# Kernel optimization log

Hardware: AMD Instinct MI355X
Metric: run time of the kernel (lower is better)

Reference implementation:

```python
import jax, jax.numpy as jnp
import numpy as np

# Transformer_E (depth=1): Residual(PreNorm(MultiScaleRetention)) + Residual1(PreNorm1(FeedForward))
# MultiScaleRetention follows the standard RetNet parallel form, adapted to two inputs
# (Q from x, K/V from z) as implied by PreNorm passing both normed streams to fn.

B, S, DIM, HEADS, MLP = 16, 1024, 256, 4, 512
HEAD = DIM // HEADS  # per-head qkv size; v_dim = DIM
EPS = 1e-5           # torch LayerNorm/GroupNorm default eps


def _ln(x, w, b):
    mu = jnp.mean(x, -1, keepdims=True)
    var = jnp.mean((x - mu) ** 2, -1, keepdims=True)
    return (x - mu) * jax.lax.rsqrt(var + EPS) * w + b


def _decay_matrix():
    # RetNet gammas: 1 - exp(linspace(log(1/32), log(1/512), heads))
    gammas = 1.0 - jnp.exp(jnp.linspace(jnp.log(1.0 / 32.0), jnp.log(1.0 / 512.0), HEADS))
    n = jnp.arange(S)
    diff = (n[:, None] - n[None, :]).astype(jnp.float32)  # [S,S]
    causal = diff >= 0
    D = jnp.where(causal[None], gammas[:, None, None] ** diff[None], 0.0)  # [H,S,S]
    return D.astype(jnp.float32)


def setup_inputs() -> dict:
    key = jax.random.key(0)
    ks = jax.random.split(key, 9)
    s = 1.0 / DIM  # repo inits W as randn/hidden_size
    return {
        "x": jax.random.normal(ks[0], (B, S, DIM), jnp.float32),
        "y": jax.random.normal(ks[1], (B, S, DIM), jnp.float32),
        "ln1_w": jnp.ones((DIM,), jnp.float32),
        "ln1_b": jnp.zeros((DIM,), jnp.float32),
        "W_Q": jax.random.normal(ks[2], (HEADS, DIM, HEAD), jnp.float32) * s,
        "W_K": jax.random.normal(ks[3], (HEADS, DIM, HEAD), jnp.float32) * s,
        "W_V": jax.random.normal(ks[4], (HEADS, DIM, HEAD), jnp.float32) * s,
        "gn_w": jnp.ones((DIM,), jnp.float32),
        "gn_b": jnp.zeros((DIM,), jnp.float32),
        "W_G": jax.random.normal(ks[5], (DIM, DIM), jnp.float32) * s,
        "W_O": jax.random.normal(ks[6], (DIM, DIM), jnp.float32) * s,
        "ln2_w": jnp.ones((DIM,), jnp.float32),
        "ln2_b": jnp.zeros((DIM,), jnp.float32),
        "ff_w1": jax.random.normal(ks[7], (DIM, MLP), jnp.float32) * (DIM ** -0.5),
        "ff_b1": jnp.zeros((MLP,), jnp.float32),
        "ff_w2": jax.random.normal(ks[8], (MLP, DIM), jnp.float32) * (MLP ** -0.5),
        "ff_b2": jnp.zeros((DIM,), jnp.float32),
    }


def reference(x, y, ln1_w, ln1_b, W_Q, W_K, W_V, gn_w, gn_b, W_G, W_O,
              ln2_w, ln2_b, ff_w1, ff_b1, ff_w2, ff_b2):
    # PreNorm: x.real -> float (already real float32 here), shared LayerNorm on both streams
    xn = _ln(x, ln1_w, ln1_b)
    zn = _ln(y, ln1_w, ln1_b)

    # --- MultiScaleRetention (parallel form) ---
    Q = jnp.einsum('bsd,hde->bhse', xn, W_Q)
    K = jnp.einsum('bsd,hde->bhse', zn, W_K)
    V = jnp.einsum('bsd,hde->bhse', zn, W_V)
    D = _decay_matrix()                                       # [H,S,S] causal decay
    scores = jnp.einsum('bhne,bhme->bhnm', Q, K) * D[None]    # [B,H,S,S]
    Yh = jnp.einsum('bhnm,bhme->bhne', scores, V)             # [B,H,S,HEAD]

    # GroupNorm(heads, v_dim) applied token-wise: normalize each head slice
    mu = jnp.mean(Yh, -1, keepdims=True)
    var = jnp.mean((Yh - mu) ** 2, -1, keepdims=True)
    Yn = (Yh - mu) * jax.lax.rsqrt(var + EPS)
    Ycat = jnp.transpose(Yn, (0, 2, 1, 3)).reshape(x.shape[0], x.shape[1], DIM)
    Ycat = Ycat * gn_w + gn_b

    # swish gate + output projection
    g = xn @ W_G
    attn_out = ((g * jax.nn.sigmoid(g)) * Ycat) @ W_O

    x1 = attn_out + x                                         # Residual

    # --- FeedForward block (Residual1(PreNorm1(FFN))) ---
    x1n = _ln(x1, ln2_w, ln2_b)
    h = jax.nn.leaky_relu(x1n @ ff_w1 + ff_b1, negative_slope=0.01)
    ff = h @ ff_w2 + ff_b2
    return ff + x1
```

## Files before the change

### kernel.cpp

```cpp
#include <hip/hip_runtime.h>

typedef float f32x4 __attribute__((ext_vector_type(4)));
typedef short bf16x8 __attribute__((ext_vector_type(8)));
typedef short s16x8 __attribute__((ext_vector_type(8)));

__device__ __forceinline__ unsigned short f2bf(float f) {
  unsigned int u = __builtin_bit_cast(unsigned int, f);
  u += 0x7fffu + ((u >> 16) & 1u);
  return (unsigned short)(u >> 16);
}
__device__ __forceinline__ float bf2f(unsigned short s) {
  unsigned int u = ((unsigned int)s) << 16;
  return __builtin_bit_cast(float, u);
}

__device__ __forceinline__ void gll16(const void* src, void* dst) {
  __builtin_amdgcn_global_load_lds((const __attribute__((address_space(1))) void*)src,
                                   (__attribute__((address_space(3))) void*)dst, 16, 0, 0);
}

__global__ __launch_bounds__(256) void prep(
    const float* __restrict__ x, const float* __restrict__ y,
    const float* __restrict__ ln1w, const float* __restrict__ ln1b,
    const float* __restrict__ WQ, const float* __restrict__ WK,
    const float* __restrict__ WV, const float* __restrict__ WG,
    const float* __restrict__ WO, const float* __restrict__ F1,
    const float* __restrict__ F2,
    unsigned short* __restrict__ XN, unsigned short* __restrict__ ZN,
    unsigned short* __restrict__ qg, unsigned short* __restrict__ kv,
    unsigned short* __restrict__ wo, unsigned short* __restrict__ f1,
    unsigned short* __restrict__ f2)
{
  const int id = blockIdx.x;
  if (id < 8192) {
    const float* X = (id < 4096) ? x : y;
    unsigned short* Y = (id < 4096) ? XN : ZN;
    const int bid = id & 4095;
    const int lane = threadIdx.x & 63;
    const size_t row = (size_t)bid * 4 + (threadIdx.x >> 6);
    const float4 v = *reinterpret_cast<const float4*>(X + row * 256 + lane * 4);
    float s = v.x + v.y + v.z + v.w;
    #pragma unroll
    for (int off = 1; off < 64; off <<= 1) s += __shfl_xor(s, off);
    float mean = s * (1.0f / 256.0f);
    float dx = v.x - mean, dy = v.y - mean, dz = v.z - mean, dw = v.w - mean;
    float q = dx * dx + dy * dy + dz * dz + dw * dw;
    #pragma unroll
    for (int off = 1; off < 64; off <<= 1) q += __shfl_xor(q, off);
    float rstd = rsqrtf(q * (1.0f / 256.0f) + 1e-5f);
    float4 wv = *reinterpret_cast<const float4*>(ln1w + lane * 4);
    float4 bv = *reinterpret_cast<const float4*>(ln1b + lane * 4);
    ushort4 o;
    o.x = f2bf(dx * rstd * wv.x + bv.x);
    o.y = f2bf(dy * rstd * wv.y + bv.y);
    o.z = f2bf(dz * rstd * wv.z + bv.z);
    o.w = f2bf(dw * rstd * wv.w + bv.w);
    *reinterpret_cast<ushort4*>(Y + row * 256 + lane * 4) = o;
    return;
  }
  int i = (id - 8192) * 256 + threadIdx.x;
  if (i < 131072) {
    int n = i >> 8, d = i & 255;
    float v = (n < 256) ? WQ[((n >> 6) * 256 + d) * 64 + (n & 63)]
                        : WG[d * 256 + (n - 256)];
    qg[i] = f2bf(v);
  } else if (i < 262144) {
    int j = i - 131072; int n = j >> 8, d = j & 255;
    float v = (n < 256) ? WK[((n >> 6) * 256 + d) * 64 + (n & 63)]
                        : WV[(((n - 256) >> 6) * 256 + d) * 64 + ((n - 256) & 63)];
    kv[j] = f2bf(v);
  } else if (i < 327680) {
    int j = i - 262144; int n = j >> 8, d = j & 255;
    wo[j] = f2bf(WO[d * 256 + n]);
  } else if (i < 458752) {
    int j = i - 327680; int n = j >> 8, d = j & 255;
    f1[j] = f2bf(F1[d * 512 + n]);
  } else if (i < 589824) {
    int j = i - 458752; int n = j >> 9, k = j & 511;
    f2[j] = f2bf(F2[k * 256 + n]);
  }
}

__global__ __launch_bounds__(256) void gemm_qkvg(
    const unsigned short* __restrict__ XN, const unsigned short* __restrict__ ZN,
    const unsigned short* __restrict__ WQG, const unsigned short* __restrict__ WKV,
    unsigned short* __restrict__ QB, unsigned short* __restrict__ GB,
    unsigned short* __restrict__ KB, unsigned short* __restrict__ VT,
    unsigned short* __restrict__ KTS)
{
  __shared__ __align__(16) char sA[2][16384];
  __shared__ __align__(16) char sB[2][8192];
  const int tid = threadIdx.x, lane = tid & 63, w = tid >> 6;
  const int z = blockIdx.z;
  const unsigned short* A = z ? ZN : XN;
  const unsigned short* Bw = z ? WKV : WQG;
  const int flat = blockIdx.x + 8 * blockIdx.y;
  const int c = flat & 7, jj = flat >> 3;
  const int m0 = (c * 16 + (jj & 15)) * 128;
  const int n0 = (jj >> 4) * 64;
  const int wr = (w >> 1) * 64, wc = (w & 1) * 32;
  const char* Ab = (const char*)A + (size_t)m0 * 512;
  const char* Bb = (const char*)Bw + (size_t)n0 * 512;
  const int srow = lane >> 3;
  const int soff = 16 * ((lane & 7) ^ srow);
  f32x4 acc[4][2] = {};

  auto stage = [&](int bufi, int kt) {
    #pragma unroll
    for (int p = 0; p < 4; ++p) {
      int row = p * 32 + w * 8 + srow;
      gll16(Ab + (size_t)row * 512 + kt + soff, &sA[bufi][p * 4096 + w * 1024]);
    }
    #pragma unroll
    for (int p = 0; p < 2; ++p) {
      int row = p * 32 + w * 8 + srow;
      gll16(Bb + (size_t)row * 512 + kt + soff, &sB[bufi][p * 4096 + w * 1024]);
    }
  };

  stage(0, 0);
  asm volatile("s_waitcnt vmcnt(0)" ::: "memory");
  __syncthreads();
  int buf = 0;
  for (int kt = 0; kt < 512; kt += 128) {
    if (kt + 128 < 512) stage(buf ^ 1, kt + 128);
    #pragma unroll
    for (int kk = 0; kk < 2; ++kk) {
      const int ib = kk * 64 + ((lane >> 4) * 16);
      bf16x8 af[4], bfr[2];
      #pragma unroll
      for (int rf = 0; rf < 4; ++rf) {
        int row = wr + rf * 16 + (lane & 15);
        af[rf] = *reinterpret_cast<const bf16x8*>(&sA[buf][row * 128 + (ib ^ ((row & 7) << 4))]);
      }
      #pragma unroll
      for (int cf = 0; cf < 2; ++cf) {
        int row = wc + cf * 16 + (lane & 15);
        bfr[cf] = *reinterpret_cast<const bf16x8*>(&sB[buf][row * 128 + (ib ^ ((row & 7) << 4))]);
      }
      #pragma unroll
      for (int rf = 0; rf < 4; ++rf)
        #pragma unroll
        for (int cf = 0; cf < 2; ++cf)
          acc[rf][cf] = __builtin_amdgcn_mfma_f32_16x16x32_bf16(af[rf], bfr[cf], acc[rf][cf], 0, 0, 0);
    }
    asm volatile("s_waitcnt vmcnt(0)" ::: "memory");
    __syncthreads();
    buf ^= 1;
  }

  const float la = logf(1.0f / 32.0f), lb = logf(1.0f / 512.0f);
  #pragma unroll
  for (int rf = 0; rf < 4; ++rf) {
    #pragma unroll
    for (int cf = 0; cf < 2; ++cf) {
      const int r0 = m0 + wr + rf * 16 + ((lane >> 4) * 4);
      const int col = n0 + wc + cf * 16 + (lane & 15);
      f32x4 v = acc[rf][cf];
      if (z == 0) {
        unsigned short* dst = (n0 < 256) ? QB : GB;
        int ccol = col & 255;
        #pragma unroll
        for (int j = 0; j < 4; ++j) dst[(size_t)(r0 + j) * 256 + ccol] = f2bf(v[j]);
      } else {
        if (n0 < 256) {
          #pragma unroll
          for (int j = 0; j < 4; ++j) KB[(size_t)(r0 + j) * 256 + col] = f2bf(v[j]);
          int hh2 = col >> 6, kd = col & 63;
          float gam = 1.0f - expf(la + (lb - la) * ((float)hh2 * (1.0f / 3.0f)));
          float lgh = log2f(gam);
          int tokc = r0 & 63;
          float scl = exp2f(lgh * (float)(64 - tokc));
          float gstep = exp2f(-lgh);
          ushort4 ks;
          ks.x = f2bf(v[0] * scl); scl *= gstep;
          ks.y = f2bf(v[1] * scl); scl *= gstep;
          ks.z = f2bf(v[2] * scl); scl *= gstep;
          ks.w = f2bf(v[3] * scl);
          int bh2 = (r0 >> 10) * 4 + hh2;
          *reinterpret_cast<ushort4*>(KTS + ((size_t)bh2 * 64 + kd) * 1024 + (r0 & 1023)) = ks;
        } else {
          int vc = col - 256, hh = vc >> 6, e = vc & 63;
          int bh = (r0 >> 10) * 4 + hh, s0 = r0 & 1023;
          ushort4 pk;
          pk.x = f2bf(v[0]); pk.y = f2bf(v[1]); pk.z = f2bf(v[2]); pk.w = f2bf(v[3]);
          *reinterpret_cast<ushort4*>(VT + (((size_t)bh * 64 + e) << 10) + s0) = pk;
        }
      }
    }
  }
}

template<int EPI>
__global__ __launch_bounds__(256) void gemm_nt(
    const unsigned short* __restrict__ A, const unsigned short* __restrict__ Bw,
    int K, unsigned short* __restrict__ o0,
    const float* __restrict__ bias, const float* __restrict__ resid,
    float* __restrict__ of)
{
  __shared__ __align__(16) char sA[2][16384];
  __shared__ __align__(16) char sB[2][8192];
  const int tid = threadIdx.x, lane = tid & 63, w = tid >> 6;
  const int flat = blockIdx.x + gridDim.x * blockIdx.y;
  const int c = flat & 7, jj = flat >> 3;
  const int m0 = (c * 16 + (jj & 15)) * 128;
  const int n0 = (jj >> 4) * 64;
  const int wr = (w >> 1) * 64, wc = (w & 1) * 32;
  const int K2 = K * 2;
  const char* Ab = (const char*)A + (size_t)m0 * K2;
  const char* Bb = (const char*)Bw + (size_t)n0 * K2;
  const int srow = lane >> 3;
  const int soff = 16 * ((lane & 7) ^ srow);
  f32x4 acc[4][2] = {};

  auto stage = [&](int bufi, int kt) {
    #pragma unroll
    for (int p = 0; p < 4; ++p) {
      int row = p * 32 + w * 8 + srow;
      gll16(Ab + (size_t)row * K2 + kt + soff, &sA[bufi][p * 4096 + w * 1024]);
    }
    #pragma unroll
    for (int p = 0; p < 2; ++p) {
      int row = p * 32 + w * 8 + srow;
      gll16(Bb + (size_t)row * K2 + kt + soff, &sB[bufi][p * 4096 + w * 1024]);
    }
  };

  stage(0, 0);
  asm volatile("s_waitcnt vmcnt(0)" ::: "memory");
  __syncthreads();
  int buf = 0;
  for (int kt = 0; kt < K2; kt += 128) {
    if (kt + 128 < K2) stage(buf ^ 1, kt + 128);
    #pragma unroll
    for (int kk = 0; kk < 2; ++kk) {
      const int ib = kk * 64 + ((lane >> 4) * 16);
      bf16x8 af[4], bfr[2];
      #pragma unroll
      for (int rf = 0; rf < 4; ++rf) {
        int row = wr + rf * 16 + (lane & 15);
        af[rf] = *reinterpret_cast<const bf16x8*>(&sA[buf][row * 128 + (ib ^ ((row & 7) << 4))]);
      }
      #pragma unroll
      for (int cf = 0; cf < 2; ++cf) {
        int row = wc + cf * 16 + (lane & 15);
        bfr[cf] = *reinterpret_cast<const bf16x8*>(&sB[buf][row * 128 + (ib ^ ((row & 7) << 4))]);
      }
      #pragma unroll
      for (int rf = 0; rf < 4; ++rf)
        #pragma unroll
        for (int cf = 0; cf < 2; ++cf)
          acc[rf][cf] = __builtin_amdgcn_mfma_f32_16x16x32_bf16(af[rf], bfr[cf], acc[rf][cf], 0, 0, 0);
    }
    asm volatile("s_waitcnt vmcnt(0)" ::: "memory");
    __syncthreads();
    buf ^= 1;
  }

  #pragma unroll
  for (int rf = 0; rf < 4; ++rf) {
    #pragma unroll
    for (int cf = 0; cf < 2; ++cf) {
      const int r0 = m0 + wr + rf * 16 + ((lane >> 4) * 4);
      const int col = n0 + wc + cf * 16 + (lane & 15);
      f32x4 v = acc[rf][cf];
      if constexpr (EPI == 3) {
        float bc = bias[col];
        #pragma unroll
        for (int j = 0; j < 4; ++j) {
          float t = v[j] + bc;
          o0[(size_t)(r0 + j) * 512 + col] = f2bf(t >= 0.0f ? t : 0.01f * t);
        }
      } else {
        float bc = bias[col];
        #pragma unroll
        for (int j = 0; j < 4; ++j) {
          size_t idx = (size_t)(r0 + j) * 256 + col;
          of[idx] = v[j] + bc + resid[idx];
        }
      }
    }
  }
}

__global__ __launch_bounds__(256) void gemm_wo_ln(
    const unsigned short* __restrict__ AY, const unsigned short* __restrict__ WoT,
    const float* __restrict__ x, const float* __restrict__ ln2w,
    const float* __restrict__ ln2b,
    float* __restrict__ X1, unsigned short* __restrict__ X1N)
{
  __shared__ __align__(16) char sA[2][4096];
  __shared__ __align__(16) char sB[2][32768];
  __shared__ float redS[32][4], redQ[32][4];
  const int tid = threadIdx.x, lane = tid & 63, w = tid >> 6;
  const int id = blockIdx.x;
  const int c = id & 7, j5 = id >> 3;
  const int m0 = (c * 64 + j5) * 32;
  const char* Ab = (const char*)AY + (size_t)m0 * 512;
  const char* Bb = (const char*)WoT;
  const int srow = lane >> 3;
  const int soff = 16 * ((lane & 7) ^ srow);
  f32x4 acc[2][4] = {};

  auto stage = [&](int bufi, int kt) {
    {
      int row = w * 8 + srow;
      gll16(Ab + (size_t)row * 512 + kt + soff, &sA[bufi][w * 1024]);
    }
    #pragma unroll
    for (int p = 0; p < 8; ++p) {
      int row = w * 64 + p * 8 + srow;
      gll16(Bb + (size_t)row * 512 + kt + soff, &sB[bufi][w * 8192 + p * 1024]);
    }
  };

  stage(0, 0);
  asm volatile("s_waitcnt vmcnt(0)" ::: "memory");
  __syncthreads();
  int buf = 0;
  for (int kt = 0; kt < 512; kt += 128) {
    if (kt + 128 < 512) stage(buf ^ 1, kt + 128);
    #pragma unroll
    for (int kk = 0; kk < 2; ++kk) {
      const int ib = kk * 64 + ((lane >> 4) * 16);
      bf16x8 af[2], bfr[4];
      #pragma unroll
      for (int mf = 0; mf < 2; ++mf) {
        int row = mf * 16 + (lane & 15);
        af[mf] = *reinterpret_cast<const bf16x8*>(&sA[buf][row * 128 + (ib ^ ((row & 7) << 4))]);
      }
      #pragma unroll
      for (int nf = 0; nf < 4; ++nf) {
        int row = w * 64 + nf * 16 + (lane & 15);
        bfr[nf] = *reinterpret_cast<const bf16x8*>(&sB[buf][row * 128 + (ib ^ ((row & 7) << 4))]);
      }
      #pragma unroll
      for (int mf = 0; mf < 2; ++mf)
        #pragma unroll
        for (int nf = 0; nf < 4; ++nf)
          acc[mf][nf] = __builtin_amdgcn_mfma_f32_16x16x32_bf16(af[mf], bfr[nf], acc[mf][nf], 0, 0, 0);
    }
    asm volatile("s_waitcnt vmcnt(0)" ::: "memory");
    __syncthreads();
    buf ^= 1;
  }

  #pragma unroll
  for (int mf = 0; mf < 2; ++mf) {
    #pragma unroll
    for (int j = 0; j < 4; ++j) {
      const int rowg = m0 + mf * 16 + ((lane >> 4) * 4) + j;
      float s = 0.0f, q = 0.0f;
      #pragma unroll
      for (int nf = 0; nf < 4; ++nf) {
        const int col = w * 64 + nf * 16 + (lane & 15);
        float v = acc[mf][nf][j] + x[(size_t)rowg * 256 + col];
        acc[mf][nf][j] = v;
        s += v; q += v * v;
      }
      #pragma unroll
      for (int off = 1; off < 16; off <<= 1) { s += __shfl_xor(s, off); q += __shfl_xor(q, off); }
      if ((lane & 15) == 0) {
        int rl = mf * 16 + ((lane >> 4) * 4) + j;
        redS[rl][w] = s; redQ[rl][w] = q;
      }
    }
  }
  __syncthreads();
  #pragma unroll
  for (int mf = 0; mf < 2; ++mf) {
    #pragma unroll
    for (int j = 0; j < 4; ++j) {
      const int rl = mf * 16 + ((lane >> 4) * 4) + j;
      const int rowg = m0 + rl;
      float sm = redS[rl][0] + redS[rl][1] + redS[rl][2] + redS[rl][3];
      float sq = redQ[rl][0] + redQ[rl][1] + redQ[rl][2] + redQ[rl][3];
      float mean = sm * (1.0f / 256.0f);
      float var = sq * (1.0f / 256.0f) - mean * mean;
      float rstd = rsqrtf(var + 1e-5f);
      #pragma unroll
      for (int nf = 0; nf < 4; ++nf) {
        const int col = w * 64 + nf * 16 + (lane & 15);
        float v = acc[mf][nf][j];
        X1[(size_t)rowg * 256 + col] = v;
        X1N[(size_t)rowg * 256 + col] = f2bf((v - mean) * rstd * ln2w[col] + ln2b[col]);
      }
    }
  }
}

__global__ __launch_bounds__(256) void calc_u(
    const unsigned short* __restrict__ KTS, const unsigned short* __restrict__ VT,
    float* __restrict__ UT)
{
  const int tid = threadIdx.x, lane = tid & 63, w = tid >> 6;
  const int id = blockIdx.x;
  const int c = id & 7, jid = id >> 3;
  const int bh = c * 8 + (jid & 7);
  const int t = jid >> 3;

  const char* Ka = (const char*)KTS +
      (((size_t)bh * 64 + w * 16 + (lane & 15)) * 1024 + t * 64 + (lane >> 4) * 8) * 2;
  const bf16x8 a0 = *reinterpret_cast<const bf16x8*>(Ka);
  const bf16x8 a1 = *reinterpret_cast<const bf16x8*>(Ka + 64);

  f32x4 c4[4] = {};
  #pragma unroll
  for (int kk = 0; kk < 2; ++kk) {
    const bf16x8 a = kk ? a1 : a0;
    #pragma unroll
    for (int cf = 0; cf < 4; ++cf) {
      const char* Vb = (const char*)VT +
          (((size_t)bh * 64 + cf * 16 + (lane & 15)) * 1024 + t * 64 + kk * 32 + (lane >> 4) * 8) * 2;
      bf16x8 bv = *reinterpret_cast<const bf16x8*>(Vb);
      c4[cf] = __builtin_amdgcn_mfma_f32_16x16x32_bf16(a, bv, c4[cf], 0, 0, 0);
    }
  }
  float* ub = UT + ((size_t)bh * 16 + t) * 4096;
  #pragma unroll
  for (int cf = 0; cf < 4; ++cf) {
    int e = cf * 16 + (lane & 15);
    *reinterpret_cast<f32x4*>(ub + e * 64 + w * 16 + (lane >> 4) * 4) = c4[cf];
  }
}

__global__ __launch_bounds__(256) void attn_ret2(
    const unsigned short* __restrict__ Qb, const unsigned short* __restrict__ Kb,
    const unsigned short* __restrict__ Vt, const unsigned short* __restrict__ Gb,
    const float* __restrict__ UT,
    const float* __restrict__ gnw, const float* __restrict__ gnb,
    unsigned short* __restrict__ AY)
{
  __shared__ __align__(16) char sK[8192];
  __shared__ __align__(16) char sV[8192];
  __shared__ __align__(16) char sP[8192];
  __shared__ __align__(16) char sS[8192];
  const int tid = threadIdx.x, lane = tid & 63, w = tid >> 6;
  const int id = blockIdx.x;
  const int c = id & 7, jid = id >> 3;
  const int bh = c * 8 + (jid & 7);
  const int qt = jid >> 3;
  const int b = bh >> 2, h = bh & 3;

  const float la = logf(1.0f / 32.0f), lb = logf(1.0f / 512.0f);
  const float gamma = 1.0f - expf(la + (lb - la) * ((float)h * (1.0f / 3.0f)));
  const float lg = log2f(gamma);

  const char* Qg = (const char*)Qb
      + ((size_t)(b * 1024 + qt * 64 + w * 16 + (lane & 15))) * 512 + h * 128 + (lane >> 4) * 16;
  const bf16x8 aq0 = *reinterpret_cast<const bf16x8*>(Qg);
  const bf16x8 aq1 = *reinterpret_cast<const bf16x8*>(Qg + 64);

  const int nloc_b = w * 16 + ((lane >> 4) * 4);
  float Aj[4], Bcf[4];
  #pragma unroll
  for (int j = 0; j < 4; ++j) Aj[j] = exp2f((float)(nloc_b + j) * lg);
  #pragma unroll
  for (int cf = 0; cf < 4; ++cf) Bcf[cf] = exp2f(-(float)(cf * 16 + (lane & 15)) * lg);

  {
    const char* kb = (const char*)Kb + ((size_t)(b * 1024 + qt * 64)) * 512 + h * 128;
    const char* vb = (const char*)Vt + ((size_t)bh * 64) * 2048 + (size_t)(qt * 64) * 2;
    const int srow = lane >> 3;
    const int soff = 16 * ((lane & 7) ^ srow);
    #pragma unroll
    for (int p = 0; p < 2; ++p) {
      int row = p * 32 + w * 8 + srow;
      gll16(kb + (size_t)row * 512 + soff, &sK[p * 4096 + w * 1024]);
      gll16(vb + (size_t)row * 2048 + soff, &sV[p * 4096 + w * 1024]);
    }
  }

  if (qt > 0) {
    f32x4 sacc[4] = {};
    float wgt = 1.0f;
    const float g64c = exp2f(64.0f * lg);
    const float* Ub = UT + ((size_t)bh * 16) * 4096;
    for (int tp = qt - 1; tp >= 0; --tp) {
      const f32x4* up = reinterpret_cast<const f32x4*>(Ub + (size_t)tp * 4096) + tid * 4;
      #pragma unroll
      for (int q = 0; q < 4; ++q) sacc[q] += up[q] * wgt;
      wgt *= g64c;
    }
    const int e = tid >> 2, kb2 = (tid & 3) * 16;
    s16x8 pk0, pk1;
    #pragma unroll
    for (int q = 0; q < 4; ++q) {
      pk0[q]     = (short)f2bf(sacc[0][q]);
      pk0[4 + q] = (short)f2bf(sacc[1][q]);
      pk1[q]     = (short)f2bf(sacc[2][q]);
      pk1[4 + q] = (short)f2bf(sacc[3][q]);
    }
    *reinterpret_cast<s16x8*>(sS + e * 128 + ((kb2 * 2) ^ ((e & 7) << 4))) = pk0;
    *reinterpret_cast<s16x8*>(sS + e * 128 + ((kb2 * 2 + 16) ^ ((e & 7) << 4))) = pk1;
  }

  asm volatile("s_waitcnt vmcnt(0)" ::: "memory");
  __syncthreads();

  f32x4 s4[4] = {};
  #pragma unroll
  for (int kk = 0; kk < 2; ++kk) {
    const int ib = kk * 64 + ((lane >> 4) * 16);
    const bf16x8 aq = kk ? aq1 : aq0;
    #pragma unroll
    for (int cf = 0; cf < 4; ++cf) {
      int kr = cf * 16 + (lane & 15);
      bf16x8 bk = *reinterpret_cast<const bf16x8*>(&sK[kr * 128 + (ib ^ ((kr & 7) << 4))]);
      s4[cf] = __builtin_amdgcn_mfma_f32_16x16x32_bf16(aq, bk, s4[cf], 0, 0, 0);
    }
  }

  #pragma unroll
  for (int cf = 0; cf < 4; ++cf) {
    const int mloc = cf * 16 + (lane & 15);
    #pragma unroll
    for (int j = 0; j < 4; ++j) {
      float p = s4[cf][j] * (Aj[j] * Bcf[cf]);
      if ((nloc_b + j - mloc) < 0) p = 0.0f;
      int pr = nloc_b + j;
      *reinterpret_cast<unsigned short*>(sP + pr * 128 + ((mloc * 2) ^ ((pr & 7) << 4))) = f2bf(p);
    }
  }

  f32x4 o[4] = {};
  #pragma unroll
  for (int kk = 0; kk < 2; ++kk) {
    const int ib = kk * 64 + ((lane >> 4) * 16);
    int pr = w * 16 + (lane & 15);
    bf16x8 ap = *reinterpret_cast<const bf16x8*>(sP + pr * 128 + (ib ^ ((pr & 7) << 4)));
    #pragma unroll
    for (int cf = 0; cf < 4; ++cf) {
      int vr = cf * 16 + (lane & 15);
      bf16x8 bv = *reinterpret_cast<const bf16x8*>(&sV[vr * 128 + (ib ^ ((vr & 7) << 4))]);
      o[cf] = __builtin_amdgcn_mfma_f32_16x16x32_bf16(ap, bv, o[cf], 0, 0, 0);
    }
  }

  if (qt > 0) {
    f32x4 ys[4] = {};
    #pragma unroll
    for (int kk = 0; kk < 2; ++kk) {
      const int ib = kk * 64 + ((lane >> 4) * 16);
      const bf16x8 aq = kk ? aq1 : aq0;
      #pragma unroll
      for (int cf = 0; cf < 4; ++cf) {
        int er = cf * 16 + (lane & 15);
        bf16x8 bs = *reinterpret_cast<const bf16x8*>(&sS[er * 128 + (ib ^ ((er & 7) << 4))]);
        ys[cf] = __builtin_amdgcn_mfma_f32_16x16x32_bf16(aq, bs, ys[cf], 0, 0, 0);
      }
    }
    #pragma unroll
    for (int cf = 0; cf < 4; ++cf)
      #pragma unroll
      for (int j = 0; j < 4; ++j) o[cf][j] += Aj[j] * ys[cf][j];
  }

  float gw[4], gb[4];
  #pragma unroll
  for (int cf = 0; cf < 4; ++cf) {
    int col = h * 64 + cf * 16 + (lane & 15);
    gw[cf] = gnw[col]; gb[cf] = gnb[col];
  }
  const int tokb = b * 1024 + qt * 64 + nloc_b;
  #pragma unroll
  for (int j = 0; j < 4; ++j) {
    float sm = 0.0f, sq = 0.0f;
    #pragma unroll
    for (int cf = 0; cf < 4; ++cf) { float xv = o[cf][j]; sm += xv; sq += xv * xv; }
    #pragma unroll
    for (int off = 1; off < 16; off <<= 1) { sm += __shfl_xor(sm, off); sq += __shfl_xor(sq, off); }
    float mean = sm * (1.0f / 64.0f);
    float var = sq * (1.0f / 64.0f) - mean * mean;
    float rstd = rsqrtf(var + 1e-5f);
    size_t tok = (size_t)(tokb + j);
    #pragma unroll
    for (int cf = 0; cf < 4; ++cf) {
      int col = h * 64 + cf * 16 + (lane & 15);
      float yn = (o[cf][j] - mean) * rstd * gw[cf] + gb[cf];
      float gv = bf2f(Gb[tok * 256 + col]);
      float sg = gv / (1.0f + expf(-gv));
      AY[tok * 256 + col] = f2bf(yn * sg);
    }
  }
}

extern "C" void kernel_launch(void* const* d_in, const int* in_sizes, int n_in,
                              void* d_out, int out_size, void* d_ws, size_t ws_size,
                              hipStream_t stream) {
  const float* x     = (const float*)d_in[0];
  const float* y     = (const float*)d_in[1];
  const float* ln1_w = (const float*)d_in[2];
  const float* ln1_b = (const float*)d_in[3];
  const float* W_Q   = (const float*)d_in[4];
  const float* W_K   = (const float*)d_in[5];
  const float* W_V   = (const float*)d_in[6];
  const float* gn_w  = (const float*)d_in[7];
  const float* gn_b  = (const float*)d_in[8];
  const float* W_G   = (const float*)d_in[9];
  const float* W_O   = (const float*)d_in[10];
  const float* ln2_w = (const float*)d_in[11];
  const float* ln2_b = (const float*)d_in[12];
  const float* ff_w1 = (const float*)d_in[13];
  const float* ff_b1 = (const float*)d_in[14];
  const float* ff_w2 = (const float*)d_in[15];
  const float* ff_b2 = (const float*)d_in[16];

  char* ws = (char*)d_ws;
  const size_t MB = 1048576;
  unsigned short* XN  = (unsigned short*)(ws + 0 * MB);
  unsigned short* ZN  = (unsigned short*)(ws + 8 * MB);
  unsigned short* QB  = (unsigned short*)(ws + 16 * MB);
  unsigned short* KB  = (unsigned short*)(ws + 24 * MB);
  unsigned short* VT  = (unsigned short*)(ws + 32 * MB);
  unsigned short* GB  = (unsigned short*)(ws + 40 * MB);
  unsigned short* WQG = (unsigned short*)(ws + 48 * MB);
  unsigned short* WKV = (unsigned short*)(ws + 48 * MB + 262144);
  unsigned short* WOp = (unsigned short*)(ws + 48 * MB + 524288);
  unsigned short* F1p = (unsigned short*)(ws + 48 * MB + 655360);
  unsigned short* F2p = (unsigned short*)(ws + 48 * MB + 917504);
  unsigned short* KTS = (unsigned short*)(ws + 56 * MB);
  float*          UT  = (float*)(ws + 64 * MB);
  float*          X1  = (float*)(ws + 16 * MB);
  unsigned short* X1N = (unsigned short*)(ws + 32 * MB);
  unsigned short* H   = (unsigned short*)(ws + 0 * MB);
  unsigned short* AY  = ZN;
  float* out = (float*)d_out;

  prep<<<10496, 256, 0, stream>>>(x, y, ln1_w, ln1_b, W_Q, W_K, W_V, W_G, W_O,
                                  ff_w1, ff_w2, XN, ZN, WQG, WKV, WOp, F1p, F2p);
  gemm_qkvg<<<dim3(8, 128, 2), 256, 0, stream>>>(XN, ZN, WQG, WKV, QB, GB, KB, VT, KTS);
  calc_u<<<1024, 256, 0, stream>>>(KTS, VT, UT);
  attn_ret2<<<1024, 256, 0, stream>>>(QB, KB, VT, GB, UT, gn_w, gn_b, AY);
  gemm_wo_ln<<<512, 256, 0, stream>>>(AY, WOp, x, ln2_w, ln2_b, X1, X1N);
  gemm_nt<3><<<dim3(8, 128), 256, 0, stream>>>(X1N, F1p, 256, H, ff_b1, nullptr, nullptr);
  gemm_nt<4><<<dim3(4, 128), 256, 0, stream>>>(H, F2p, 512, nullptr, ff_b2, X1, out);
}
```

Baseline: 105.2 us.

## Compute chunked retention state prefix-scan in dedicated kernel, store decayed K once

Replaces the per-chunk U computation and the per-query-tile fp32 summation loop over prior chunks with a calc_s kernel that scans the 16 chunks sequentially and writes a bf16 inter-chunk state per chunk. The attention kernel then loads that state straight into LDS through global_load_lds instead of re-summing up to 15 fp32 U tiles. K is stored pre-scaled by the decay in a chunk-tiled layout, and the intra-chunk score scaling drops one factor. The trade-off is that calc_s runs only 128 blocks with a serial 15-step loop, so it exposes little parallelism, and the bf16 state and pre-scaled K add rounding error.

```diff
diff --git a/kernel.cpp b/kernel.cpp
--- a/kernel.cpp
+++ b/kernel.cpp
@@ -2,7 +2,6 @@
 
 typedef float f32x4 __attribute__((ext_vector_type(4)));
 typedef short bf16x8 __attribute__((ext_vector_type(8)));
-typedef short s16x8 __attribute__((ext_vector_type(8)));
 
 __device__ __forceinline__ unsigned short f2bf(float f) {
   unsigned int u = __builtin_bit_cast(unsigned int, f);
@@ -86,7 +85,7 @@
     const unsigned short* __restrict__ WQG, const unsigned short* __restrict__ WKV,
     unsigned short* __restrict__ QB, unsigned short* __restrict__ GB,
     unsigned short* __restrict__ KB, unsigned short* __restrict__ VT,
-    unsigned short* __restrict__ KTS)
+    unsigned short* __restrict__ KTT)
 {
   __shared__ __align__(16) char sA[2][16384];
   __shared__ __align__(16) char sB[2][8192];
@@ -149,7 +148,15 @@
     buf ^= 1;
   }
 
-  const float la = logf(1.0f / 32.0f), lb = logf(1.0f / 512.0f);
+  float lgh = 0.0f, gstep = 0.0f;
+  if (z == 1 && n0 < 256) {
+    const float la = logf(1.0f / 32.0f), lb = logf(1.0f / 512.0f);
+    const int hh2 = n0 >> 6;
+    float gam = 1.0f - expf(la + (lb - la) * ((float)hh2 * (1.0f / 3.0f)));
+    lgh = log2f(gam);
+    gstep = exp2f(-lgh);
+  }
+
   #pragma unroll
   for (int rf = 0; rf < 4; ++rf) {
     #pragma unroll
@@ -164,21 +171,20 @@
         for (int j = 0; j < 4; ++j) dst[(size_t)(r0 + j) * 256 + ccol] = f2bf(v[j]);
       } else {
         if (n0 < 256) {
-          #pragma unroll
-          for (int j = 0; j < 4; ++j) KB[(size_t)(r0 + j) * 256 + col] = f2bf(v[j]);
-          int hh2 = col >> 6, kd = col & 63;
-          float gam = 1.0f - expf(la + (lb - la) * ((float)hh2 * (1.0f / 3.0f)));
-          float lgh = log2f(gam);
-          int tokc = r0 & 63;
+          const int tokc = r0 & 63, t2 = (r0 & 1023) >> 6, kd = col & 63;
+          const int bh2 = (r0 >> 10) * 4 + (n0 >> 6);
           float scl = exp2f(lgh * (float)(64 - tokc));
-          float gstep = exp2f(-lgh);
           ushort4 ks;
-          ks.x = f2bf(v[0] * scl); scl *= gstep;
-          ks.y = f2bf(v[1] * scl); scl *= gstep;
-          ks.z = f2bf(v[2] * scl); scl *= gstep;
-          ks.w = f2bf(v[3] * scl);
-          int bh2 = (r0 >> 10) * 4 + hh2;
-          *reinterpret_cast<ushort4*>(KTS + ((size_t)bh2 * 64 + kd) * 1024 + (r0 & 1023)) = ks;
+          float s0v = v[0] * scl; scl *= gstep;
+          float s1v = v[1] * scl; scl *= gstep;
+          float s2v = v[2] * scl; scl *= gstep;
+          float s3v = v[3] * scl;
+          ks.x = f2bf(s0v); ks.y = f2bf(s1v); ks.z = f2bf(s2v); ks.w = f2bf(s3v);
+          KB[(size_t)(r0 + 0) * 256 + col] = ks.x;
+          KB[(size_t)(r0 + 1) * 256 + col] = ks.y;
+          KB[(size_t)(r0 + 2) * 256 + col] = ks.z;
+          KB[(size_t)(r0 + 3) * 256 + col] = ks.w;
+          *reinterpret_cast<ushort4*>(KTT + (((size_t)bh2 * 16 + t2) * 64 + kd) * 64 + tokc) = ks;
         } else {
           int vc = col - 256, hh = vc >> 6, e = vc & 63;
           int bh = (r0 >> 10) * 4 + hh, s0 = r0 & 1023;
@@ -389,52 +395,62 @@
   }
 }
 
-__global__ __launch_bounds__(256) void calc_u(
-    const unsigned short* __restrict__ KTS, const unsigned short* __restrict__ VT,
-    float* __restrict__ UT)
+__global__ __launch_bounds__(256) void calc_s(
+    const unsigned short* __restrict__ KTT, const unsigned short* __restrict__ VT,
+    unsigned short* __restrict__ SB)
 {
   const int tid = threadIdx.x, lane = tid & 63, w = tid >> 6;
-  const int id = blockIdx.x;
-  const int c = id & 7, jid = id >> 3;
-  const int bh = c * 8 + (jid & 7);
-  const int t = jid >> 3;
-
-  const char* Ka = (const char*)KTS +
-      (((size_t)bh * 64 + w * 16 + (lane & 15)) * 1024 + t * 64 + (lane >> 4) * 8) * 2;
-  const bf16x8 a0 = *reinterpret_cast<const bf16x8*>(Ka);
-  const bf16x8 a1 = *reinterpret_cast<const bf16x8*>(Ka + 64);
-
-  f32x4 c4[4] = {};
-  #pragma unroll
-  for (int kk = 0; kk < 2; ++kk) {
-    const bf16x8 a = kk ? a1 : a0;
-    #pragma unroll
-    for (int cf = 0; cf < 4; ++cf) {
-      const char* Vb = (const char*)VT +
-          (((size_t)bh * 64 + cf * 16 + (lane & 15)) * 1024 + t * 64 + kk * 32 + (lane >> 4) * 8) * 2;
-      bf16x8 bv = *reinterpret_cast<const bf16x8*>(Vb);
-      c4[cf] = __builtin_amdgcn_mfma_f32_16x16x32_bf16(a, bv, c4[cf], 0, 0, 0);
-    }
-  }
-  float* ub = UT + ((size_t)bh * 16 + t) * 4096;
-  #pragma unroll
-  for (int cf = 0; cf < 4; ++cf) {
-    int e = cf * 16 + (lane & 15);
-    *reinterpret_cast<f32x4*>(ub + e * 64 + w * 16 + (lane >> 4) * 4) = c4[cf];
+  const int bh = blockIdx.x >> 1, eh = blockIdx.x & 1;
+  const int h = bh & 3;
+  const float la = logf(1.0f / 32.0f), lb = logf(1.0f / 512.0f);
+  const float gamma = 1.0f - expf(la + (lb - la) * ((float)h * (1.0f / 3.0f)));
+  const float g64 = exp2f(64.0f * log2f(gamma));
+
+  const char* Kbase = (const char*)KTT + (size_t)bh * 16 * 4096 * 2;
+  const char* Vbase = (const char*)VT + (size_t)bh * 64 * 1024 * 2;
+  f32x4 S[2] = {};
+
+  for (int t = 0; t < 15; ++t) {
+    f32x4 U[2] = {};
+    #pragma unroll
+    for (int kk = 0; kk < 2; ++kk) {
+      const bf16x8 a = *reinterpret_cast<const bf16x8*>(
+          Kbase + (((size_t)t * 64 + w * 16 + (lane & 15)) * 64 + kk * 32 + (lane >> 4) * 8) * 2);
+      #pragma unroll
+      for (int cf = 0; cf < 2; ++cf) {
+        const int e = eh * 32 + cf * 16 + (lane & 15);
+        const bf16x8 bv = *reinterpret_cast<const bf16x8*>(
+            Vbase + (((size_t)e) * 1024 + t * 64 + kk * 32 + (lane >> 4) * 8) * 2);
+        U[cf] = __builtin_amdgcn_mfma_f32_16x16x32_bf16(a, bv, U[cf], 0, 0, 0);
+      }
+    }
+    #pragma unroll
+    for (int cf = 0; cf < 2; ++cf)
+      #pragma unroll
+      for (int q = 0; q < 4; ++q) S[cf][q] = S[cf][q] * g64 + U[cf][q];
+    const int k0 = w * 16 + ((lane >> 4) * 4);
+    #pragma unroll
+    for (int cf = 0; cf < 2; ++cf) {
+      const int e = eh * 32 + cf * 16 + (lane & 15);
+      ushort4 pk;
+      pk.x = f2bf(S[cf][0]); pk.y = f2bf(S[cf][1]);
+      pk.z = f2bf(S[cf][2]); pk.w = f2bf(S[cf][3]);
+      *reinterpret_cast<ushort4*>(SB + (((size_t)bh * 16 + t + 1) * 64 + e) * 64 + k0) = pk;
+    }
   }
 }
 
 __global__ __launch_bounds__(256) void attn_ret2(
-    const unsigned short* __restrict__ Qb, const unsigned short* __restrict__ Kb,
+    const unsigned short* __restrict__ Qb, const unsigned short* __restrict__ Kt,
     const unsigned short* __restrict__ Vt, const unsigned short* __restrict__ Gb,
-    const float* __restrict__ UT,
+    const unsigned short* __restrict__ SB,
     const float* __restrict__ gnw, const float* __restrict__ gnb,
     unsigned short* __restrict__ AY)
 {
   __shared__ __align__(16) char sK[8192];
   __shared__ __align__(16) char sV[8192];
+  __shared__ __align__(16) char sS[8192];
   __shared__ __align__(16) char sP[8192];
-  __shared__ __align__(16) char sS[8192];
   const int tid = threadIdx.x, lane = tid & 63, w = tid >> 6;
   const int id = blockIdx.x;
   const int c = id & 7, jid = id >> 3;
@@ -452,14 +468,16 @@
   const bf16x8 aq1 = *reinterpret_cast<const bf16x8*>(Qg + 64);
 
   const int nloc_b = w * 16 + ((lane >> 4) * 4);
-  float Aj[4], Bcf[4];
-  #pragma unroll
-  for (int j = 0; j < 4; ++j) Aj[j] = exp2f((float)(nloc_b + j) * lg);
-  #pragma unroll
-  for (int cf = 0; cf < 4; ++cf) Bcf[cf] = exp2f(-(float)(cf * 16 + (lane & 15)) * lg);
+  float Aj[4], Ajm[4];
+  const float g64i = exp2f(-64.0f * lg);
+  #pragma unroll
+  for (int j = 0; j < 4; ++j) {
+    Aj[j] = exp2f((float)(nloc_b + j) * lg);
+    Ajm[j] = Aj[j] * g64i;
+  }
 
   {
-    const char* kb = (const char*)Kb + ((size_t)(b * 1024 + qt * 64)) * 512 + h * 128;
+    const char* kb = (const char*)Kt + ((size_t)(b * 1024 + qt * 64)) * 512 + h * 128;
     const char* vb = (const char*)Vt + ((size_t)bh * 64) * 2048 + (size_t)(qt * 64) * 2;
     const int srow = lane >> 3;
     const int soff = 16 * ((lane & 7) ^ srow);
@@ -469,32 +487,15 @@
       gll16(kb + (size_t)row * 512 + soff, &sK[p * 4096 + w * 1024]);
       gll16(vb + (size_t)row * 2048 + soff, &sV[p * 4096 + w * 1024]);
     }
-  }
-
-  if (qt > 0) {
-    f32x4 sacc[4] = {};
-    float wgt = 1.0f;
-    const float g64c = exp2f(64.0f * lg);
-    const float* Ub = UT + ((size_t)bh * 16) * 4096;
-    for (int tp = qt - 1; tp >= 0; --tp) {
-      const f32x4* up = reinterpret_cast<const f32x4*>(Ub + (size_t)tp * 4096) + tid * 4;
-      #pragma unroll
-      for (int q = 0; q < 4; ++q) sacc[q] += up[q] * wgt;
-      wgt *= g64c;
-    }
-    const int e = tid >> 2, kb2 = (tid & 3) * 16;
-    s16x8 pk0, pk1;
-    #pragma unroll
-    for (int q = 0; q < 4; ++q) {
-      pk0[q]     = (short)f2bf(sacc[0][q]);
-      pk0[4 + q] = (short)f2bf(sacc[1][q]);
-      pk1[q]     = (short)f2bf(sacc[2][q]);
-      pk1[4 + q] = (short)f2bf(sacc[3][q]);
-    }
-    *reinterpret_cast<s16x8*>(sS + e * 128 + ((kb2 * 2) ^ ((e & 7) << 4))) = pk0;
-    *reinterpret_cast<s16x8*>(sS + e * 128 + ((kb2 * 2 + 16) ^ ((e & 7) << 4))) = pk1;
-  }
-
+    if (qt > 0) {
+      const char* sb = (const char*)SB + (((size_t)bh * 16 + qt) * 4096) * 2;
+      #pragma unroll
+      for (int p = 0; p < 2; ++p) {
+        int row = p * 32 + w * 8 + srow;
+        gll16(sb + (size_t)row * 128 + soff, &sS[p * 4096 + w * 1024]);
+      }
+    }
+  }
   asm volatile("s_waitcnt vmcnt(0)" ::: "memory");
   __syncthreads();
 
@@ -516,7 +517,7 @@
     const int mloc = cf * 16 + (lane & 15);
     #pragma unroll
     for (int j = 0; j < 4; ++j) {
-      float p = s4[cf][j] * (Aj[j] * Bcf[cf]);
+      float p = s4[cf][j] * Ajm[j];
       if ((nloc_b + j - mloc) < 0) p = 0.0f;
       int pr = nloc_b + j;
       *reinterpret_cast<unsigned short*>(sP + pr * 128 + ((mloc * 2) ^ ((pr & 7) << 4))) = f2bf(p);
@@ -619,8 +620,8 @@
   unsigned short* WOp = (unsigned short*)(ws + 48 * MB + 524288);
   unsigned short* F1p = (unsigned short*)(ws + 48 * MB + 655360);
   unsigned short* F2p = (unsigned short*)(ws + 48 * MB + 917504);
-  unsigned short* KTS = (unsigned short*)(ws + 56 * MB);
-  float*          UT  = (float*)(ws + 64 * MB);
+  unsigned short* KTT = (unsigned short*)(ws + 56 * MB);
+  unsigned short* SB  = (unsigned short*)(ws + 64 * MB);
   float*          X1  = (float*)(ws + 16 * MB);
   unsigned short* X1N = (unsigned short*)(ws + 32 * MB);
   unsigned short* H   = (unsigned short*)(ws + 0 * MB);
@@ -629,9 +630,9 @@
 
   prep<<<10496, 256, 0, stream>>>(x, y, ln1_w, ln1_b, W_Q, W_K, W_V, W_G, W_O,
                                   ff_w1, ff_w2, XN, ZN, WQG, WKV, WOp, F1p, F2p);
-  gemm_qkvg<<<dim3(8, 128, 2), 256, 0, stream>>>(XN, ZN, WQG, WKV, QB, GB, KB, VT, KTS);
-  calc_u<<<1024, 256, 0, stream>>>(KTS, VT, UT);
-  attn_ret2<<<1024, 256, 0, stream>>>(QB, KB, VT, GB, UT, gn_w, gn_b, AY);
+  gemm_qkvg<<<dim3(8, 128, 2), 256, 0, stream>>>(XN, ZN, WQG, WKV, QB, GB, KB, VT, KTT);
+  calc_s<<<128, 256, 0, stream>>>(KTT, VT, SB);
+  attn_ret2<<<1024, 256, 0, stream>>>(QB, KB, VT, GB, SB, gn_w, gn_b, AY);
   gemm_wo_ln<<<512, 256, 0, stream>>>(AY, WOp, x, ln2_w, ln2_b, X1, X1N);
   gemm_nt<3><<<dim3(8, 128), 256, 0, stream>>>(X1N, F1p, 256, H, ff_b1, nullptr, nullptr);
   gemm_nt<4><<<dim3(4, 128), 256, 0, stream>>>(H, F2p, 512, nullptr, ff_b2, X1, out);
```

After: 110.5 us. 5.0% more time.
